# Kernel tuning notes

Hardware: AMD Instinct MI355X
Metric: run time of the kernel (lower is better)

## Reference

```python
import jax, jax.numpy as jnp
import numpy as np

B, T, D = 4, 4096, 1024

def setup_inputs() -> dict:
    key = jax.random.key(0)
    kx, kq, kk, kv = jax.random.split(key, 4)
    s = 1.0 / np.sqrt(D)
    return {
        "x": jax.random.normal(kx, (B, T, D), dtype=jnp.float32),
        "Wq": jax.random.normal(kq, (D, D), dtype=jnp.float32) * s,
        "Wk": jax.random.normal(kk, (D, D), dtype=jnp.float32) * s,
        "Wv": jax.random.normal(kv, (D, D), dtype=jnp.float32) * s,
    }

def reference(x, Wq, Wk, Wv):
    # x: [B, T, D]; W*: [D, D] (torch Linear weight, y = x @ W.T)
    Q = jnp.einsum("btd,ed->bte", x, Wq)
    K = jnp.einsum("btd,ed->bte", x, Wk)
    V = jnp.einsum("btd,ed->bte", x, Wv)
    scale = jnp.asarray(np.sqrt(D), dtype=x.dtype)
    scores = jnp.einsum("bqd,bkd->bqk", Q, K) / scale  # [B, T, T]
    weights = jax.nn.softmax(scores, axis=-1)
    return jnp.einsum("bqk,bkd->bqd", weights, V)
```

## Files before the change

### kernel.cpp

```cpp
#include <hip/hip_runtime.h>
#include <stdint.h>

typedef unsigned short u16;
typedef __attribute__((ext_vector_type(4))) float f32x4;
typedef __attribute__((ext_vector_type(8))) short s16x8;

#define TB 4
#define TT 4096
#define TD 1024

__device__ __forceinline__ u16 f2bf(float f) {
  union { float f; uint32_t u; } v; v.f = f;
  return (u16)((v.u + 0x7FFFu + ((v.u >> 16) & 1u)) >> 16);
}
__device__ __forceinline__ float bf2f(u16 h) {
  union { uint32_t u; float f; } v; v.u = ((uint32_t)h) << 16;
  return v.f;
}

#define GLOAD_LDS16(g, l) __builtin_amdgcn_global_load_lds( \
    (const __attribute__((address_space(1))) void*)(g),      \
    (__attribute__((address_space(3))) void*)(l), 16, 0, 0)

#define MFMA16(a, b, c) __builtin_amdgcn_mfma_f32_16x16x32_bf16(a, b, c, 0, 0, 0)
#define LDSV(o) (*(const s16x8*)&ls[(o)])

__global__ void cast_all(const float* __restrict__ x, const float* __restrict__ wq,
                         const float* __restrict__ wk, const float* __restrict__ wv,
                         u16* __restrict__ dst) {
  const int NX = 1 << 22;
  const int NW = 1 << 18;
  const int NT = NX + 3 * NW;
  int i = blockIdx.x * blockDim.x + threadIdx.x;
  int stride = gridDim.x * blockDim.x;
  for (; i < NT; i += stride) {
    float4 v;
    if (i < NX) {
      v = ((const float4*)x)[i];
    } else {
      int j = i - NX;
      int w = j >> 18;
      int off = j & (NW - 1);
      const float* p = (w == 0) ? wq : (w == 1) ? wk : wv;
      v = ((const float4*)p)[off];
    }
    ushort4 o;
    o.x = f2bf(v.x); o.y = f2bf(v.y); o.z = f2bf(v.z); o.w = f2bf(v.w);
    ((ushort4*)dst)[i] = o;
  }
}

template<bool OUT_BF16>
__global__ __launch_bounds__(512)
void gemm256(const u16* __restrict__ Abase, const u16* __restrict__ Bt,
             void* __restrict__ C, int K, int lda, int ldb, int ldc,
             float s0, float s1,
             size_t oA0, size_t oA1, size_t oA2, size_t oA3, size_t sB,
             size_t oC0, size_t oC1, size_t oC2, size_t oC3) {
  __shared__ u16 ls[65536];
  const int tid  = threadIdx.x;
  const int lane = tid & 63;
  const int wid  = tid >> 6;
  const int wm   = wid >> 2;
  const int wn   = wid & 3;

  const int nxy = gridDim.x * gridDim.y;
  const int id  = blockIdx.y * gridDim.x + blockIdx.x;
  const int sid = (id & 7) * (nxy >> 3) + (id >> 3);
  const int bx  = sid % gridDim.x;
  const int by  = sid / gridDim.x;
  const int brow = by * 256;
  const int bcol = bx * 256;

  const int z = blockIdx.z;
  const size_t oA = (z == 0) ? oA0 : (z == 1) ? oA1 : (z == 2) ? oA2 : oA3;
  const size_t oC = (z == 0) ? oC0 : (z == 1) ? oC1 : (z == 2) ? oC2 : oC3;
  const float scale = (z == 0) ? s0 : s1;
  const u16* A = Abase + oA;
  Bt += (size_t)z * sB;

  const int lr = lane >> 3;
  const int lc = (lane & 7) ^ lr;

  auto STAGE_BLK = [&](int slotB, int kt, int op, int r0) {
    const u16* g = op ? (Bt + (size_t)bcol * ldb) : (A + (size_t)brow * lda);
    const int ld = op ? ldb : lda;
    const int r  = r0 + wid * 8 + lr;
    GLOAD_LDS16(g + (size_t)r * ld + (size_t)kt * 64 + (size_t)lc * 8,
                &ls[slotB + op * 16384 + (r0 + wid * 8) * 64]);
  };

  f32x4 acc[8][4];
#pragma unroll
  for (int m = 0; m < 8; ++m)
#pragma unroll
    for (int n = 0; n < 4; ++n) acc[m][n] = (f32x4){0.f, 0.f, 0.f, 0.f};

  const int nt = K >> 6;

  STAGE_BLK(0, 0, 0, 0);   STAGE_BLK(0, 0, 0, 64);
  STAGE_BLK(0, 0, 0, 128); STAGE_BLK(0, 0, 0, 192);
  STAGE_BLK(0, 0, 1, 0);   STAGE_BLK(0, 0, 1, 64);
  STAGE_BLK(0, 0, 1, 128); STAGE_BLK(0, 0, 1, 192);
  if (nt > 1) {
    STAGE_BLK(32768, 1, 1, 0);   STAGE_BLK(32768, 1, 1, 64);
    STAGE_BLK(32768, 1, 1, 128); STAGE_BLK(32768, 1, 1, 192);
    STAGE_BLK(32768, 1, 0, 0);   STAGE_BLK(32768, 1, 0, 128);
    asm volatile("s_waitcnt vmcnt(6)" ::: "memory");
  } else {
    asm volatile("s_waitcnt vmcnt(0)" ::: "memory");
  }
  __builtin_amdgcn_s_barrier();

  const int r16 = lane & 15;
  const int k8  = lane >> 4;
  const int sw  = r16 & 7;
  const int c0  = ((k8)     ^ sw) * 8;
  const int c1  = ((4 | k8) ^ sw) * 8;
  int aBase[8], bBase[4];
#pragma unroll
  for (int m = 0; m < 8; ++m) aBase[m] = (wm * 128 + m * 16 + r16) * 64;
#pragma unroll
  for (int n = 0; n < 4; ++n) bBase[n] = 16384 + (wn * 64 + n * 16 + r16) * 64;

  s16x8 bf[4][2], af_x[2][2], af_y[2][2];

#define READ_APAIR(DST, SB, M0)                               \
  DST[0][0] = LDSV((SB) + aBase[M0] + c0);                    \
  DST[0][1] = LDSV((SB) + aBase[M0] + c1);                    \
  DST[1][0] = LDSV((SB) + aBase[(M0) + 1] + c0);              \
  DST[1][1] = LDSV((SB) + aBase[(M0) + 1] + c1);

#define READ_B(SB)                                            \
  _Pragma("unroll")                                           \
  for (int n = 0; n < 4; ++n) {                               \
    bf[n][0] = LDSV((SB) + bBase[n] + c0);                    \
    bf[n][1] = LDSV((SB) + bBase[n] + c1);                    \
  }

#define CLUSTER(MB, AF)                                                  \
  __builtin_amdgcn_s_setprio(1);                                         \
  _Pragma("unroll")                                                      \
  for (int mm = 0; mm < 2; ++mm)                                         \
    _Pragma("unroll")                                                    \
    for (int n = 0; n < 4; ++n) {                                        \
      acc[(MB) + mm][n] = MFMA16(AF[mm][0], bf[n][0], acc[(MB) + mm][n]); \
      acc[(MB) + mm][n] = MFMA16(AF[mm][1], bf[n][1], acc[(MB) + mm][n]); \
    }                                                                    \
  __builtin_amdgcn_s_setprio(0);

  READ_B(0);
  READ_APAIR(af_x, 0, 0);

  for (int t = 0; t < nt; ++t) {
    const int sb  = (t & 1) << 15;
    const int sbn = sb ^ 32768;
    const bool pf1 = (t + 1 < nt);
    const bool pf2 = (t + 2 < nt);

    if (pf1) { STAGE_BLK(sbn, t + 1, 0, 64); STAGE_BLK(sbn, t + 1, 0, 192); }
    READ_APAIR(af_y, sb, 2);
    CLUSTER(0, af_x);
    __builtin_amdgcn_s_barrier();

    if (pf2) { STAGE_BLK(sb, t + 2, 1, 0); STAGE_BLK(sb, t + 2, 1, 64); }
    READ_APAIR(af_x, sb, 4);
    CLUSTER(2, af_y);
    __builtin_amdgcn_s_barrier();

    if (pf2) { STAGE_BLK(sb, t + 2, 1, 128); STAGE_BLK(sb, t + 2, 1, 192); }
    READ_APAIR(af_y, sb, 6);
    CLUSTER(4, af_x);
    if (pf2) asm volatile("s_waitcnt vmcnt(4)" ::: "memory");
    else     asm volatile("s_waitcnt vmcnt(0)" ::: "memory");
    __builtin_amdgcn_s_barrier();

    if (pf2) { STAGE_BLK(sb, t + 2, 0, 0); STAGE_BLK(sb, t + 2, 0, 128); }
    CLUSTER(6, af_y);
    if (pf1) { READ_B(sbn); READ_APAIR(af_x, sbn, 0); }
    __builtin_amdgcn_s_barrier();
  }
#undef READ_APAIR
#undef READ_B
#undef CLUSTER

  const int c16 = lane & 15;
  const int rhi = lane >> 4;
#pragma unroll
  for (int m = 0; m < 8; ++m)
#pragma unroll
    for (int n = 0; n < 4; ++n)
#pragma unroll
      for (int r = 0; r < 4; ++r) {
        int grow = brow + wm * 128 + m * 16 + rhi * 4 + r;
        int gcol = bcol + wn * 64 + n * 16 + c16;
        float v = acc[m][n][r] * scale;
        if (OUT_BF16) ((u16*)C)[oC + (size_t)grow * ldc + gcol] = f2bf(v);
        else          ((float*)C)[oC + (size_t)grow * ldc + gcol] = v;
      }
}

__global__ __launch_bounds__(256)
void transpose_bf16(const u16* __restrict__ V, u16* __restrict__ Vt) {
  __shared__ u16 tile[64][65];
  int b  = blockIdx.z;
  int t0 = blockIdx.y * 64;
  int e0 = blockIdx.x * 64;
  const u16* Vb  = V  + (size_t)b * TT * TD;
  u16*       Vtb = Vt + (size_t)b * TT * TD;
  int r  = threadIdx.x >> 4;
  int c4 = threadIdx.x & 15;
#pragma unroll
  for (int i = 0; i < 4; ++i) {
    int row = r + i * 16;
    ushort4 v = *(const ushort4*)&Vb[(size_t)(t0 + row) * TD + e0 + c4 * 4];
    tile[row][c4 * 4 + 0] = v.x;
    tile[row][c4 * 4 + 1] = v.y;
    tile[row][c4 * 4 + 2] = v.z;
    tile[row][c4 * 4 + 3] = v.w;
  }
  __syncthreads();
#pragma unroll
  for (int i = 0; i < 4; ++i) {
    int e = r + i * 16;
    ushort4 o;
    o.x = tile[c4 * 4 + 0][e];
    o.y = tile[c4 * 4 + 1][e];
    o.z = tile[c4 * 4 + 2][e];
    o.w = tile[c4 * 4 + 3][e];
    *(ushort4*)&Vtb[(size_t)(e0 + e) * TT + t0 + c4 * 4] = o;
  }
}

__global__ __launch_bounds__(256)
void softmax4(u16* __restrict__ p0, u16* __restrict__ p1,
              u16* __restrict__ p2, u16* __restrict__ p3) {
  __shared__ float red_m[4];
  __shared__ float red_s[4];
  const int bi = blockIdx.x >> 12;
  u16* base = (bi == 0) ? p0 : (bi == 1) ? p1 : (bi == 2) ? p2 : p3;
  const int row = blockIdx.x & 4095;
  int tid  = threadIdx.x;
  int lane = tid & 63;
  int wid  = tid >> 6;
  s16x8* Sr = (s16x8*)(base + (size_t)row * 4096);

  float v[16];
  float m = -1e30f;
#pragma unroll
  for (int i = 0; i < 2; ++i) {
    s16x8 u = Sr[tid + i * 256];
#pragma unroll
    for (int j = 0; j < 8; ++j) {
      v[i * 8 + j] = bf2f((u16)u[j]);
      m = fmaxf(m, v[i * 8 + j]);
    }
  }
#pragma unroll
  for (int off = 32; off >= 1; off >>= 1) m = fmaxf(m, __shfl_xor(m, off));
  if (lane == 0) red_m[wid] = m;
  __syncthreads();
  m = fmaxf(fmaxf(red_m[0], red_m[1]), fmaxf(red_m[2], red_m[3]));

  float s = 0.f;
#pragma unroll
  for (int j = 0; j < 16; ++j) { v[j] = __expf(v[j] - m); s += v[j]; }
#pragma unroll
  for (int off = 32; off >= 1; off >>= 1) s += __shfl_xor(s, off);
  if (lane == 0) red_s[wid] = s;
  __syncthreads();
  s = red_s[0] + red_s[1] + red_s[2] + red_s[3];
  float inv = 1.0f / s;

#pragma unroll
  for (int i = 0; i < 2; ++i) {
    s16x8 o;
#pragma unroll
    for (int j = 0; j < 8; ++j) o[j] = (short)f2bf(v[i * 8 + j] * inv);
    Sr[tid + i * 256] = o;
  }
}

extern "C" void kernel_launch(void* const* d_in, const int* in_sizes, int n_in,
                              void* d_out, int out_size, void* d_ws, size_t ws_size,
                              hipStream_t stream) {
  const float* x  = (const float*)d_in[0];
  const float* Wq = (const float*)d_in[1];
  const float* Wk = (const float*)d_in[2];
  const float* Wv = (const float*)d_in[3];
  float* out = (float*)d_out;

  const size_t MT = (size_t)TB * TT;
  const size_t BE = (size_t)TT * TD;
  const size_t XE = MT * TD;
  const size_t WE = (size_t)TD * TD;

  u16* xb   = (u16*)d_ws;
  u16* wqb  = xb + XE;
  u16* Q    = wqb + 3 * WE;
  u16* Kb   = Q + XE;
  u16* Vt   = Kb + XE;
  u16* PB   = Vt + XE;
  u16* tmpS = PB + 2 * XE;

  cast_all<<<2048, 256, 0, stream>>>(x, Wq, Wk, Wv, xb);

  dim3 blk(512);
  gemm256<true><<<dim3(TD / 256, MT / 256, 3), blk, 0, stream>>>(
      xb, wqb, Q, TD, TD, TD, TD, 0.03125f, 1.0f,
      0, 0, 0, 0, WE,
      0, XE, (size_t)(PB - Q), 0);

  transpose_bf16<<<dim3(TD / 64, TT / 64, TB), 256, 0, stream>>>(PB, Vt);

  gemm256<true><<<dim3(TT / 256, TT / 256, TB), blk, 0, stream>>>(
      Q, Kb, xb, TD, TD, TD, TT, 1.0f, 1.0f,
      0, BE, 2 * BE, 3 * BE, BE,
      0, (size_t)(PB - xb), (size_t)(PB + XE - xb), (size_t)(tmpS - xb));

  softmax4<<<dim3(TB * TT), 256, 0, stream>>>(xb, PB, PB + XE, tmpS);

  gemm256<false><<<dim3(TD / 256, TT / 256, TB), blk, 0, stream>>>(
      xb, Vt, out, TT, TT, TT, TD, 1.0f, 1.0f,
      0, (size_t)(PB - xb), (size_t)(PB + XE - xb), (size_t)(tmpS - xb), BE,
      0, BE, 2 * BE, 3 * BE);
}
```

Baseline: 438.8 us.

## Restructure GEMM main loop into 8-phase ping-pong schedule with quadrant MFMA clusters

Replaces the per-k-tile 4-cluster loop with a loop unrolled over two k-tiles. Each tile is split into four 4x2 MFMA quadrant clusters, each preceded by LDS fragment reads and half-tile global-to-LDS prefetches, and pinned with sched_barrier plus s_barrier. The aim is to interleave loads and MFMA more evenly and improve overlap, at the cost of more barriers per tile. It assumes an even number of k-tiles (nt>>1), so odd K would be mishandled.

```diff
diff --git a/kernel.cpp b/kernel.cpp
--- a/kernel.cpp
+++ b/kernel.cpp
@@ -82,13 +82,17 @@
   const int lr = lane >> 3;
   const int lc = (lane & 7) ^ lr;
 
-  auto STAGE_BLK = [&](int slotB, int kt, int op, int r0) {
+  auto SBLK = [&](int slotB, int kt, int op, int r0) {
     const u16* g = op ? (Bt + (size_t)bcol * ldb) : (A + (size_t)brow * lda);
     const int ld = op ? ldb : lda;
     const int r  = r0 + wid * 8 + lr;
     GLOAD_LDS16(g + (size_t)r * ld + (size_t)kt * 64 + (size_t)lc * 8,
                 &ls[slotB + op * 16384 + (r0 + wid * 8) * 64]);
   };
+  auto SHALF = [&](int slotB, int kt, int op, int h) {
+    SBLK(slotB, kt, op, h * 128);
+    SBLK(slotB, kt, op, h * 128 + 64);
+  };
 
   f32x4 acc[8][4];
 #pragma unroll
@@ -97,19 +101,12 @@
     for (int n = 0; n < 4; ++n) acc[m][n] = (f32x4){0.f, 0.f, 0.f, 0.f};
 
   const int nt = K >> 6;
-
-  STAGE_BLK(0, 0, 0, 0);   STAGE_BLK(0, 0, 0, 64);
-  STAGE_BLK(0, 0, 0, 128); STAGE_BLK(0, 0, 0, 192);
-  STAGE_BLK(0, 0, 1, 0);   STAGE_BLK(0, 0, 1, 64);
-  STAGE_BLK(0, 0, 1, 128); STAGE_BLK(0, 0, 1, 192);
-  if (nt > 1) {
-    STAGE_BLK(32768, 1, 1, 0);   STAGE_BLK(32768, 1, 1, 64);
-    STAGE_BLK(32768, 1, 1, 128); STAGE_BLK(32768, 1, 1, 192);
-    STAGE_BLK(32768, 1, 0, 0);   STAGE_BLK(32768, 1, 0, 128);
-    asm volatile("s_waitcnt vmcnt(6)" ::: "memory");
-  } else {
-    asm volatile("s_waitcnt vmcnt(0)" ::: "memory");
-  }
+  const int NI = nt >> 1;
+
+  SHALF(0, 0, 0, 0); SHALF(0, 0, 0, 1);
+  SHALF(0, 0, 1, 0); SHALF(0, 0, 1, 1);
+  SHALF(32768, 1, 1, 0); SHALF(32768, 1, 1, 1);
+  asm volatile("s_waitcnt vmcnt(4)" ::: "memory");
   __builtin_amdgcn_s_barrier();
 
   const int r16 = lane & 15;
@@ -123,66 +120,93 @@
 #pragma unroll
   for (int n = 0; n < 4; ++n) bBase[n] = 16384 + (wn * 64 + n * 16 + r16) * 64;
 
-  s16x8 bf[4][2], af_x[2][2], af_y[2][2];
-
-#define READ_APAIR(DST, SB, M0)                               \
-  DST[0][0] = LDSV((SB) + aBase[M0] + c0);                    \
-  DST[0][1] = LDSV((SB) + aBase[M0] + c1);                    \
-  DST[1][0] = LDSV((SB) + aBase[(M0) + 1] + c0);              \
-  DST[1][1] = LDSV((SB) + aBase[(M0) + 1] + c1);
-
-#define READ_B(SB)                                            \
-  _Pragma("unroll")                                           \
-  for (int n = 0; n < 4; ++n) {                               \
-    bf[n][0] = LDSV((SB) + bBase[n] + c0);                    \
-    bf[n][1] = LDSV((SB) + bBase[n] + c1);                    \
-  }
-
-#define CLUSTER(MB, AF)                                                  \
-  __builtin_amdgcn_s_setprio(1);                                         \
-  _Pragma("unroll")                                                      \
-  for (int mm = 0; mm < 2; ++mm)                                         \
-    _Pragma("unroll")                                                    \
-    for (int n = 0; n < 4; ++n) {                                        \
-      acc[(MB) + mm][n] = MFMA16(AF[mm][0], bf[n][0], acc[(MB) + mm][n]); \
-      acc[(MB) + mm][n] = MFMA16(AF[mm][1], bf[n][1], acc[(MB) + mm][n]); \
-    }                                                                    \
+  s16x8 af[4][2], bf[4][2];
+
+#define READ_A4(SB, MH)                                                        \
+  af[0][0] = LDSV((SB) + aBase[(MH)*4+0] + c0); af[0][1] = LDSV((SB) + aBase[(MH)*4+0] + c1); \
+  af[1][0] = LDSV((SB) + aBase[(MH)*4+1] + c0); af[1][1] = LDSV((SB) + aBase[(MH)*4+1] + c1); \
+  af[2][0] = LDSV((SB) + aBase[(MH)*4+2] + c0); af[2][1] = LDSV((SB) + aBase[(MH)*4+2] + c1); \
+  af[3][0] = LDSV((SB) + aBase[(MH)*4+3] + c0); af[3][1] = LDSV((SB) + aBase[(MH)*4+3] + c1);
+
+#define READ_B2(SB, N0)                                                        \
+  bf[(N0)  ][0] = LDSV((SB) + bBase[(N0)  ] + c0); bf[(N0)  ][1] = LDSV((SB) + bBase[(N0)  ] + c1); \
+  bf[(N0)+1][0] = LDSV((SB) + bBase[(N0)+1] + c0); bf[(N0)+1][1] = LDSV((SB) + bBase[(N0)+1] + c1);
+
+#define CLUST(MH, NH)                                                          \
+  __builtin_amdgcn_s_setprio(1);                                               \
+  _Pragma("unroll")                                                            \
+  for (int mm = 0; mm < 4; ++mm) {                                             \
+    _Pragma("unroll")                                                          \
+    for (int nn = 0; nn < 2; ++nn) {                                           \
+      acc[(MH)*4+mm][(NH)*2+nn] =                                              \
+          MFMA16(af[mm][0], bf[(NH)*2+nn][0], acc[(MH)*4+mm][(NH)*2+nn]);      \
+      acc[(MH)*4+mm][(NH)*2+nn] =                                              \
+          MFMA16(af[mm][1], bf[(NH)*2+nn][1], acc[(MH)*4+mm][(NH)*2+nn]);      \
+    }                                                                          \
+  }                                                                            \
   __builtin_amdgcn_s_setprio(0);
 
-  READ_B(0);
-  READ_APAIR(af_x, 0, 0);
-
-  for (int t = 0; t < nt; ++t) {
-    const int sb  = (t & 1) << 15;
-    const int sbn = sb ^ 32768;
-    const bool pf1 = (t + 1 < nt);
-    const bool pf2 = (t + 2 < nt);
-
-    if (pf1) { STAGE_BLK(sbn, t + 1, 0, 64); STAGE_BLK(sbn, t + 1, 0, 192); }
-    READ_APAIR(af_y, sb, 2);
-    CLUSTER(0, af_x);
-    __builtin_amdgcn_s_barrier();
-
-    if (pf2) { STAGE_BLK(sb, t + 2, 1, 0); STAGE_BLK(sb, t + 2, 1, 64); }
-    READ_APAIR(af_x, sb, 4);
-    CLUSTER(2, af_y);
-    __builtin_amdgcn_s_barrier();
-
-    if (pf2) { STAGE_BLK(sb, t + 2, 1, 128); STAGE_BLK(sb, t + 2, 1, 192); }
-    READ_APAIR(af_y, sb, 6);
-    CLUSTER(4, af_x);
-    if (pf2) asm volatile("s_waitcnt vmcnt(4)" ::: "memory");
-    else     asm volatile("s_waitcnt vmcnt(0)" ::: "memory");
-    __builtin_amdgcn_s_barrier();
-
-    if (pf2) { STAGE_BLK(sb, t + 2, 0, 0); STAGE_BLK(sb, t + 2, 0, 128); }
-    CLUSTER(6, af_y);
-    if (pf1) { READ_B(sbn); READ_APAIR(af_x, sbn, 0); }
-    __builtin_amdgcn_s_barrier();
-  }
-#undef READ_APAIR
-#undef READ_B
-#undef CLUSTER
+#define PIN() __builtin_amdgcn_sched_barrier(0)
+#define BAR() __builtin_amdgcn_s_barrier()
+
+  for (int i = 0; i < NI; ++i) {
+    const int t1 = 2 * i + 1, t2 = 2 * i + 2, t3 = 2 * i + 3;
+    const bool p2 = t2 < nt, p3 = t3 < nt;
+
+    READ_A4(0, 0); READ_B2(0, 0);
+    SHALF(32768, t1, 0, 0);
+    PIN(); BAR();
+    CLUST(0, 0);
+    BAR();
+
+    READ_B2(0, 2);
+    SHALF(32768, t1, 0, 1);
+    PIN(); BAR();
+    CLUST(0, 1);
+    BAR();
+
+    READ_A4(0, 1);
+    if (p2) SHALF(0, t2, 1, 0);
+    PIN(); BAR();
+    CLUST(1, 0);
+    BAR();
+
+    if (p2) SHALF(0, t2, 1, 1);
+    PIN(); BAR();
+    CLUST(1, 1);
+    if (p2) asm volatile("s_waitcnt vmcnt(4)" ::: "memory");
+    else    asm volatile("s_waitcnt vmcnt(0)" ::: "memory");
+    BAR();
+
+    READ_A4(32768, 0); READ_B2(32768, 0);
+    if (p2) SHALF(0, t2, 0, 0);
+    PIN(); BAR();
+    CLUST(0, 0);
+    BAR();
+
+    READ_B2(32768, 2);
+    if (p2) SHALF(0, t2, 0, 1);
+    PIN(); BAR();
+    CLUST(0, 1);
+    BAR();
+
+    READ_A4(32768, 1);
+    if (p3) SHALF(32768, t3, 1, 0);
+    PIN(); BAR();
+    CLUST(1, 0);
+    BAR();
+
+    if (p3) SHALF(32768, t3, 1, 1);
+    PIN(); BAR();
+    CLUST(1, 1);
+    if (i + 1 < NI) asm volatile("s_waitcnt vmcnt(4)" ::: "memory");
+    BAR();
+  }
+#undef READ_A4
+#undef READ_B2
+#undef CLUST
+#undef PIN
+#undef BAR
 
   const int c16 = lane & 15;
   const int rhi = lane >> 4;
```

Measured after the change: 432.3 us. No clear change (-1.5%).
